# Kernel optimization log

Hardware: AMD Instinct MI355X
Metric: run time of the kernel (lower is better)

## Reference

```python
import jax, jax.numpy as jnp
import numpy as np
from jax import lax

N_ITERS = 50
SIGMA = 1e-6
RHO_MIN, RHO_MAX = 1e-6, 1e6


def _chol_solve(L, b):
    # Solve M x = b given M = L L^T (batched lower-triangular L)
    y = lax.linalg.triangular_solve(L, b, left_side=True, lower=True)
    return lax.linalg.triangular_solve(L, y, left_side=True, lower=True, transpose_a=True)


def setup_inputs() -> dict:
    key = jax.random.key(0)
    kq, kp, ka = jax.random.split(key, 3)
    B, n_x, n_A = 128, 512, 512
    G = jax.random.normal(kq, (B, n_x, n_x), dtype=jnp.float32)
    # SPD quadratic term, as required by the QP solver
    Q = jnp.matmul(G, jnp.swapaxes(G, 1, 2)) / n_x + 0.1 * jnp.eye(n_x, dtype=jnp.float32)
    p = 0.1 * jax.random.normal(kp, (B, n_x, 1), dtype=jnp.float32)
    A = jax.random.normal(ka, (B, n_A, n_x), dtype=jnp.float32) / np.sqrt(n_x).astype(np.float32)
    lb = -jnp.ones((B, n_A, 1), dtype=jnp.float32)
    ub = jnp.ones((B, n_A, 1), dtype=jnp.float32)
    return {"Q": Q, "p": p, "A": A, "lb": lb, "ub": ub}


def reference(Q, p, A, lb, ub):
    B, n_A, n_x = A.shape
    AT = jnp.swapaxes(A, 1, 2)                      # [B, n_x, n_A]
    ATA = jnp.matmul(AT, A)                         # [B, n_x, n_x]

    # rho heuristic from scqpth_solve (Frobenius matrix norms), held constant
    A_norm = jnp.linalg.norm(ATA, axis=(1, 2), keepdims=True)
    Q_norm = jnp.linalg.norm(Q, axis=(1, 2), keepdims=True)
    rho = (Q_norm / A_norm) * (n_A / n_x) ** 0.5    # [B,1,1]
    rho = jnp.clip(rho, RHO_MIN, RHO_MAX)
    rho = lax.stop_gradient(rho)

    M = Q + rho * ATA + SIGMA * jnp.eye(n_x, dtype=Q.dtype)
    L = jnp.linalg.cholesky(M)                      # factor once (M is SPD)

    x0 = jnp.zeros((B, n_x, 1), dtype=Q.dtype)
    z0 = jnp.zeros((B, n_A, 1), dtype=Q.dtype)
    u0 = jnp.zeros((B, n_A, 1), dtype=Q.dtype)

    def step(carry, _):
        x, z, u = carry
        rhs = -p + rho * jnp.matmul(AT, z - u) + SIGMA * x
        x = _chol_solve(L, rhs)
        Ax = jnp.matmul(A, x)
        z = jnp.clip(Ax + u, lb, ub)                # projection onto [lb, ub]
        u = u + Ax - z                              # scaled dual update
        return (x, z, u), None

    (x, z, u), _ = lax.scan(step, (x0, z0, u0), None, length=N_ITERS)
    return x
```

## Files before the change

kernel.cpp:

```cpp
#include <hip/hip_runtime.h>

#define NBATCH 128
#define NDIM 512
static constexpr size_t MAT = (size_t)NDIM * NDIM;
static constexpr size_t BATMAT = (size_t)NBATCH * MAT;
#define SIGMA_F 1e-6f

template <int TA, int TB>
__global__ __launch_bounds__(256) void gemm512b(const float* __restrict__ Ag,
                                                const float* __restrict__ Bg,
                                                float* __restrict__ Cg,
                                                const float* __restrict__ alphaPtr) {
  const int b = blockIdx.z;
  const float* Ab = Ag + (size_t)b * MAT;
  const float* Bb = Bg + (size_t)b * MAT;
  float* Cb = Cg + (size_t)b * MAT;
  const int i0 = blockIdx.y * 128, j0 = blockIdx.x * 128;
  __shared__ float As[32][132];
  __shared__ float Bs[32][132];
  const int tid = threadIdx.x;
  const int tx = tid & 15, ty = tid >> 4;
  float acc[2][2][4][4] = {};
  for (int k0 = 0; k0 < NDIM; k0 += 32) {
    if (TA == 0) {
      const int kk = tid >> 5, c4 = (tid & 31) << 2;
#pragma unroll
      for (int pp = 0; pp < 4; ++pp) {
        float4 v = *reinterpret_cast<const float4*>(&Ab[(size_t)(k0 + kk + 8 * pp) * NDIM + i0 + c4]);
        *reinterpret_cast<float4*>(&As[kk + 8 * pp][c4]) = v;
      }
    } else {
      const int m = tid >> 3, kq = (tid & 7) << 2;
#pragma unroll
      for (int pp = 0; pp < 4; ++pp) {
        float4 v = *reinterpret_cast<const float4*>(&Ab[(size_t)(i0 + m + 32 * pp) * NDIM + k0 + kq]);
        As[kq + 0][m + 32 * pp] = v.x;
        As[kq + 1][m + 32 * pp] = v.y;
        As[kq + 2][m + 32 * pp] = v.z;
        As[kq + 3][m + 32 * pp] = v.w;
      }
    }
    if (TB == 0) {
      const int kk = tid >> 5, c4 = (tid & 31) << 2;
#pragma unroll
      for (int pp = 0; pp < 4; ++pp) {
        float4 v = *reinterpret_cast<const float4*>(&Bb[(size_t)(k0 + kk + 8 * pp) * NDIM + j0 + c4]);
        *reinterpret_cast<float4*>(&Bs[kk + 8 * pp][c4]) = v;
      }
    } else {
      const int m = tid >> 3, kq = (tid & 7) << 2;
#pragma unroll
      for (int pp = 0; pp < 4; ++pp) {
        float4 v = *reinterpret_cast<const float4*>(&Bb[(size_t)(j0 + m + 32 * pp) * NDIM + k0 + kq]);
        Bs[kq + 0][m + 32 * pp] = v.x;
        Bs[kq + 1][m + 32 * pp] = v.y;
        Bs[kq + 2][m + 32 * pp] = v.z;
        Bs[kq + 3][m + 32 * pp] = v.w;
      }
    }
    __syncthreads();
#pragma unroll
    for (int kk = 0; kk < 32; ++kk) {
      float4 a0 = *reinterpret_cast<const float4*>(&As[kk][ty << 2]);
      float4 a1 = *reinterpret_cast<const float4*>(&As[kk][64 + (ty << 2)]);
      float4 b0 = *reinterpret_cast<const float4*>(&Bs[kk][tx << 2]);
      float4 b1 = *reinterpret_cast<const float4*>(&Bs[kk][64 + (tx << 2)]);
      const float ar[2][4] = {{a0.x, a0.y, a0.z, a0.w}, {a1.x, a1.y, a1.z, a1.w}};
      const float br[2][4] = {{b0.x, b0.y, b0.z, b0.w}, {b1.x, b1.y, b1.z, b1.w}};
#pragma unroll
      for (int ri = 0; ri < 2; ++ri)
#pragma unroll
        for (int ci = 0; ci < 2; ++ci)
#pragma unroll
          for (int r = 0; r < 4; ++r)
#pragma unroll
            for (int c = 0; c < 4; ++c)
              acc[ri][ci][r][c] += ar[ri][r] * br[ci][c];
    }
    __syncthreads();
  }
  const float alpha = alphaPtr ? alphaPtr[b] : 1.0f;
#pragma unroll
  for (int ri = 0; ri < 2; ++ri)
#pragma unroll
    for (int r = 0; r < 4; ++r) {
      const int gi = i0 + ri * 64 + (ty << 2) + r;
#pragma unroll
      for (int ci = 0; ci < 2; ++ci) {
        float4 o = make_float4(alpha * acc[ri][ci][r][0], alpha * acc[ri][ci][r][1],
                               alpha * acc[ri][ci][r][2], alpha * acc[ri][ci][r][3]);
        *reinterpret_cast<float4*>(&Cb[(size_t)gi * NDIM + j0 + ci * 64 + (tx << 2)]) = o;
      }
    }
}

__global__ __launch_bounds__(512) void norms_rho(const float* __restrict__ Q,
                                                 const float* __restrict__ ATA,
                                                 float* __restrict__ rho) {
  const int b = blockIdx.x;
  const int tid = threadIdx.x;
  const float* Qb = Q + (size_t)b * MAT;
  const float* Tb = ATA + (size_t)b * MAT;
  double sq = 0.0, st = 0.0;
  for (int e = tid; e < (int)MAT; e += 512) {
    float q = Qb[e];
    float t = Tb[e];
    sq += (double)q * q;
    st += (double)t * t;
  }
  __shared__ double s1[512];
  __shared__ double s2[512];
  s1[tid] = sq;
  s2[tid] = st;
  __syncthreads();
  for (int h = 256; h > 0; h >>= 1) {
    if (tid < h) {
      s1[tid] += s1[tid + h];
      s2[tid] += s2[tid + h];
    }
    __syncthreads();
  }
  if (tid == 0) {
    double r = sqrt(s1[0]) / sqrt(s2[0]);
    r = fmin(fmax(r, 1e-6), 1e6);
    rho[b] = (float)r;
  }
}

__global__ void form_m(const float* __restrict__ Q, const float* __restrict__ rho,
                       float* __restrict__ M) {
  size_t stride = (size_t)gridDim.x * blockDim.x;
  for (size_t e = (size_t)blockIdx.x * blockDim.x + threadIdx.x; e < BATMAT; e += stride) {
    int b = (int)(e >> 18);
    int ij = (int)(e & (MAT - 1));
    int i = ij >> 9, j = ij & 511;
    float v = Q[e] + rho[b] * M[e];
    if (i == j) v += SIGMA_F;
    M[e] = v;
  }
}

__global__ __launch_bounds__(256) void gj_pivot(float* __restrict__ Mg,
                                                float* __restrict__ Csave, int p) {
  const int b = blockIdx.x;
  float* M = Mg + (size_t)b * MAT;
  float* Cs = Csave + (size_t)b * ((size_t)NDIM * 64);
  const int tid = threadIdx.x;
  const int k0 = p * 64;
  for (int e = tid; e < 512 * 16; e += 256) {
    int r = e >> 4, c4 = (e & 15) << 2;
    float4 v = *reinterpret_cast<const float4*>(&M[(size_t)r * NDIM + k0 + c4]);
    *reinterpret_cast<float4*>(&Cs[r * 64 + c4]) = v;
  }
  const int r = tid & 63, cb = (tid >> 6) << 4;
  float dreg[16];
#pragma unroll
  for (int q = 0; q < 16; ++q) dreg[q] = M[(size_t)(k0 + r) * NDIM + k0 + cb + q];
  __shared__ float rowb[64];
  __shared__ float colb[64];
  for (int j = 0; j < 64; ++j) {
    const int jc = j - cb;
    if (jc >= 0 && jc < 16) colb[r] = dreg[jc];
    if (r == j) {
#pragma unroll
      for (int q = 0; q < 16; ++q) rowb[cb + q] = dreg[q];
    }
    __syncthreads();
    const float piv = 1.0f / rowb[j];
    const float cj = colb[r];
    if (r == j) {
#pragma unroll
      for (int q = 0; q < 16; ++q) dreg[q] = (cb + q == j) ? piv : rowb[cb + q] * piv;
    } else {
#pragma unroll
      for (int q = 0; q < 16; ++q) {
        float rv = rowb[cb + q] * piv;
        dreg[q] = (cb + q == j) ? (-cj * piv) : fmaf(-cj, rv, dreg[q]);
      }
    }
    __syncthreads();
  }
#pragma unroll
  for (int q = 0; q < 16; ++q) M[(size_t)(k0 + r) * NDIM + k0 + cb + q] = dreg[q];
}

__global__ __launch_bounds__(256) void gj_row(float* __restrict__ Mg, int p) {
  const int b = blockIdx.y;
  const int jt = blockIdx.x + (blockIdx.x >= p ? 1 : 0);
  float* M = Mg + (size_t)b * MAT;
  const int k0 = p * 64, j0 = jt * 64;
  __shared__ float Ss[64][68];
  __shared__ float Rs[64][68];
  const int tid = threadIdx.x;
  for (int e = tid; e < 1024; e += 256) {
    int rr = e >> 4, c4 = (e & 15) << 2;
    *reinterpret_cast<float4*>(&Ss[rr][c4]) =
        *reinterpret_cast<const float4*>(&M[(size_t)(k0 + rr) * NDIM + k0 + c4]);
    *reinterpret_cast<float4*>(&Rs[rr][c4]) =
        *reinterpret_cast<const float4*>(&M[(size_t)(k0 + rr) * NDIM + j0 + c4]);
  }
  __syncthreads();
  const int tx = tid & 15, ty = tid >> 4;
  float acc[4][4] = {};
#pragma unroll 16
  for (int m = 0; m < 64; ++m) {
    float4 a = *reinterpret_cast<const float4*>(&Ss[m][ty << 2]);
    float4 bv = *reinterpret_cast<const float4*>(&Rs[m][tx << 2]);
    acc[0][0] += a.x * bv.x; acc[0][1] += a.x * bv.y; acc[0][2] += a.x * bv.z; acc[0][3] += a.x * bv.w;
    acc[1][0] += a.y * bv.x; acc[1][1] += a.y * bv.y; acc[1][2] += a.y * bv.z; acc[1][3] += a.y * bv.w;
    acc[2][0] += a.z * bv.x; acc[2][1] += a.z * bv.y; acc[2][2] += a.z * bv.z; acc[2][3] += a.z * bv.w;
    acc[3][0] += a.w * bv.x; acc[3][1] += a.w * bv.y; acc[3][2] += a.w * bv.z; acc[3][3] += a.w * bv.w;
  }
#pragma unroll
  for (int rr = 0; rr < 4; ++rr) {
    float4 o = make_float4(acc[rr][0], acc[rr][1], acc[rr][2], acc[rr][3]);
    *reinterpret_cast<float4*>(&M[(size_t)(k0 + (ty << 2) + rr) * NDIM + j0 + (tx << 2)]) = o;
  }
}

__global__ __launch_bounds__(256) void gj_update(float* __restrict__ Mg,
                                                 const float* __restrict__ Csave, int p) {
  const int b = blockIdx.z;
  const int jt = blockIdx.x;
  const int it = blockIdx.y + (blockIdx.y >= p ? 1 : 0);
  float* M = Mg + (size_t)b * MAT;
  const float* Cs = Csave + (size_t)b * ((size_t)NDIM * 64);
  const int k0 = p * 64, i0 = it * 64, j0 = jt * 64;
  __shared__ float Ts[64][68];
  __shared__ float Rs[64][68];
  const int tid = threadIdx.x;
  {
    const int rr = tid >> 2, mq = (tid & 3) << 4;
#pragma unroll
    for (int q = 0; q < 4; ++q) {
      float4 v = *reinterpret_cast<const float4*>(&Cs[(i0 + rr) * 64 + mq + q * 4]);
      Ts[mq + q * 4 + 0][rr] = v.x;
      Ts[mq + q * 4 + 1][rr] = v.y;
      Ts[mq + q * 4 + 2][rr] = v.z;
      Ts[mq + q * 4 + 3][rr] = v.w;
    }
  }
  for (int e = tid; e < 1024; e += 256) {
    int rr = e >> 4, c4 = (e & 15) << 2;
    *reinterpret_cast<float4*>(&Rs[rr][c4]) =
        *reinterpret_cast<const float4*>(&M[(size_t)(k0 + rr) * NDIM + j0 + c4]);
  }
  __syncthreads();
  const int tx = tid & 15, ty = tid >> 4;
  float acc[4][4] = {};
#pragma unroll 16
  for (int m = 0; m < 64; ++m) {
    float4 a = *reinterpret_cast<const float4*>(&Ts[m][ty << 2]);
    float4 bv = *reinterpret_cast<const float4*>(&Rs[m][tx << 2]);
    acc[0][0] += a.x * bv.x; acc[0][1] += a.x * bv.y; acc[0][2] += a.x * bv.z; acc[0][3] += a.x * bv.w;
    acc[1][0] += a.y * bv.x; acc[1][1] += a.y * bv.y; acc[1][2] += a.y * bv.z; acc[1][3] += a.y * bv.w;
    acc[2][0] += a.z * bv.x; acc[2][1] += a.z * bv.y; acc[2][2] += a.z * bv.z; acc[2][3] += a.z * bv.w;
    acc[3][0] += a.w * bv.x; acc[3][1] += a.w * bv.y; acc[3][2] += a.w * bv.z; acc[3][3] += a.w * bv.w;
  }
  if (jt == p) {
#pragma unroll
    for (int rr = 0; rr < 4; ++rr) {
      float4 o = make_float4(-acc[rr][0], -acc[rr][1], -acc[rr][2], -acc[rr][3]);
      *reinterpret_cast<float4*>(&M[(size_t)(i0 + (ty << 2) + rr) * NDIM + j0 + (tx << 2)]) = o;
    }
  } else {
#pragma unroll
    for (int rr = 0; rr < 4; ++rr) {
      float* dst = &M[(size_t)(i0 + (ty << 2) + rr) * NDIM + j0 + (tx << 2)];
      float4 cur = *reinterpret_cast<const float4*>(dst);
      cur.x -= acc[rr][0];
      cur.y -= acc[rr][1];
      cur.z -= acc[rr][2];
      cur.w -= acc[rr][3];
      *reinterpret_cast<float4*>(dst) = cur;
    }
  }
}

__global__ __launch_bounds__(512) void cvec_kernel(const float* __restrict__ Minv,
                                                   const float* __restrict__ p,
                                                   float* __restrict__ c) {
  const int b = blockIdx.x, i = threadIdx.x;
  __shared__ float ps[512];
  ps[i] = p[b * NDIM + i];
  __syncthreads();
  const float* Mb = Minv + (size_t)b * MAT;
  float acc = 0.f;
#pragma unroll 8
  for (int m = 0; m < NDIM; ++m) acc += Mb[m * NDIM + i] * ps[m];
  c[b * NDIM + i] = -acc;
}

__global__ __launch_bounds__(512) void dvec_kernel(const float* __restrict__ Ain,
                                                   const float* __restrict__ c,
                                                   float* __restrict__ d) {
  const int b = blockIdx.x, i = threadIdx.x;
  __shared__ float cs[512];
  cs[i] = c[b * NDIM + i];
  __syncthreads();
  const int wv = i >> 6, ln = i & 63;
  const float* Ab = Ain + (size_t)b * MAT;
  for (int q = 0; q < 64; ++q) {
    const int j = wv * 64 + q;
    const float* Arow = Ab + (size_t)j * NDIM;
    float s = 0.f;
#pragma unroll
    for (int h = 0; h < 8; ++h) s += Arow[h * 64 + ln] * cs[h * 64 + ln];
    for (int off = 32; off > 0; off >>= 1) s += __shfl_down(s, off);
    if (ln == 0) d[b * NDIM + j] = s;
  }
}

__global__ __launch_bounds__(512) void admm_step(const float* __restrict__ S,
                                                 const float* __restrict__ dvec,
                                                 const float* __restrict__ lb,
                                                 const float* __restrict__ ub,
                                                 float* __restrict__ wbuf,
                                                 float* __restrict__ ubuf) {
  const int blk = blockIdx.x;
  const int b = blk >> 1, h = blk & 1;
  const int t = threadIdx.x;
  __shared__ float ws_s[512];
  __shared__ float4 part[512];
  ws_s[t] = wbuf[b * NDIM + t];
  __syncthreads();
  const int j4 = t & 63;
  const int ks = t >> 6;
  const float4* Srow = reinterpret_cast<const float4*>(S + (size_t)b * MAT) +
                       (size_t)(ks * 64) * 128 + h * 64 + j4;
  float4 acc = make_float4(0.f, 0.f, 0.f, 0.f);
#pragma unroll 8
  for (int k = 0; k < 64; ++k) {
    float w = ws_s[ks * 64 + k];
    float4 s = Srow[(size_t)k * 128];
    acc.x += s.x * w;
    acc.y += s.y * w;
    acc.z += s.z * w;
    acc.w += s.w * w;
  }
  part[t] = acc;
  __syncthreads();
  if (t < 64) {
    float4 y = part[t];
#pragma unroll
    for (int s = 1; s < 8; ++s) {
      float4 q = part[s * 64 + t];
      y.x += q.x; y.y += q.y; y.z += q.z; y.w += q.w;
    }
    const size_t off = (size_t)b * NDIM + h * 256 + t * 4;
    float4 dv = *reinterpret_cast<const float4*>(dvec + off);
    float4 uv = *reinterpret_cast<const float4*>(ubuf + off);
    float4 lbv = *reinterpret_cast<const float4*>(lb + off);
    float4 ubv = *reinterpret_cast<const float4*>(ub + off);
    y.x += dv.x; y.y += dv.y; y.z += dv.z; y.w += dv.w;
    float4 zv, wv;
    zv.x = fminf(fmaxf(y.x + uv.x, lbv.x), ubv.x);
    zv.y = fminf(fmaxf(y.y + uv.y, lbv.y), ubv.y);
    zv.z = fminf(fmaxf(y.z + uv.z, lbv.z), ubv.z);
    zv.w = fminf(fmaxf(y.w + uv.w, lbv.w), ubv.w);
    uv.x += y.x - zv.x; uv.y += y.y - zv.y; uv.z += y.z - zv.z; uv.w += y.w - zv.w;
    wv.x = zv.x - uv.x; wv.y = zv.y - uv.y; wv.z = zv.z - uv.z; wv.w = zv.w - uv.w;
    *reinterpret_cast<float4*>(ubuf + off) = uv;
    *reinterpret_cast<float4*>(wbuf + off) = wv;
  }
}

__global__ __launch_bounds__(512) void final_x(const float* __restrict__ P1,
                                               const float* __restrict__ c,
                                               const float* __restrict__ w,
                                               float* __restrict__ out) {
  const int b = blockIdx.x, i = threadIdx.x;
  __shared__ float ws_s[512];
  ws_s[i] = w[b * NDIM + i];
  __syncthreads();
  const float* Pb = P1 + (size_t)b * MAT;
  float acc = 0.f;
#pragma unroll 8
  for (int k = 0; k < NDIM; ++k) acc += Pb[(size_t)k * NDIM + i] * ws_s[k];
  out[b * NDIM + i] = c[b * NDIM + i] + acc;
}

extern "C" void kernel_launch(void* const* d_in, const int* in_sizes, int n_in,
                              void* d_out, int out_size, void* d_ws, size_t ws_size,
                              hipStream_t stream) {
  const float* Q = (const float*)d_in[0];
  const float* p = (const float*)d_in[1];
  const float* A = (const float*)d_in[2];
  const float* lb = (const float*)d_in[3];
  const float* ub = (const float*)d_in[4];
  float* out = (float*)d_out;

  float* B0 = (float*)d_ws;
  float* B1 = B0 + BATMAT;
  float* cbuf = B1 + BATMAT;
  float* dbuf = cbuf + NBATCH * NDIM;
  float* wbuf = dbuf + NBATCH * NDIM;
  float* ubuf = wbuf + NBATCH * NDIM;
  float* rhobuf = ubuf + NBATCH * NDIM;

  hipMemsetAsync(wbuf, 0, 2 * NBATCH * NDIM * sizeof(float), stream);

  gemm512b<0, 0><<<dim3(4, 4, NBATCH), 256, 0, stream>>>(A, A, B0, nullptr);
  norms_rho<<<NBATCH, 512, 0, stream>>>(Q, B0, rhobuf);
  form_m<<<2048, 256, 0, stream>>>(Q, rhobuf, B0);
  for (int p8 = 0; p8 < 8; ++p8) {
    gj_pivot<<<NBATCH, 256, 0, stream>>>(B0, B1, p8);
    gj_row<<<dim3(7, NBATCH), 256, 0, stream>>>(B0, p8);
    gj_update<<<dim3(8, 7, NBATCH), 256, 0, stream>>>(B0, B1, p8);
  }
  cvec_kernel<<<NBATCH, 512, 0, stream>>>(B0, p, cbuf);
  gemm512b<1, 0><<<dim3(4, 4, NBATCH), 256, 0, stream>>>(A, B0, B1, rhobuf);
  dvec_kernel<<<NBATCH, 512, 0, stream>>>(A, cbuf, dbuf);
  gemm512b<1, 1><<<dim3(4, 4, NBATCH), 256, 0, stream>>>(B1, A, B0, nullptr);
  for (int it = 0; it < 49; ++it)
    admm_step<<<2 * NBATCH, 512, 0, stream>>>(B0, dbuf, lb, ub, wbuf, ubuf);
  final_x<<<NBATCH, 512, 0, stream>>>(B1, cbuf, wbuf, out);
}
```

Before: 4.399 ms.

## Use split-bf16 MFMA for batched GEMMs and widen ADMM step grid

Replaces the FP32 SIMT batched GEMM with an MFMA kernel. Each FP32 operand is split into high and low bf16 parts, and three bf16 products are accumulated to approximate FP32 accuracy. The rho scaling moves from the second GEMM to the third GEMM and to final_x. The per-iteration ADMM step is split into four blocks per batch instead of two, to raise parallelism across the GPU. This adds conversion overhead and slightly lower precision in exchange for matrix-core throughput.

```diff
diff --git a/kernel.cpp b/kernel.cpp
--- a/kernel.cpp
+++ b/kernel.cpp
@@ -6,91 +6,129 @@
 static constexpr size_t BATMAT = (size_t)NBATCH * MAT;
 #define SIGMA_F 1e-6f
 
-template <int TA, int TB>
-__global__ __launch_bounds__(256) void gemm512b(const float* __restrict__ Ag,
-                                                const float* __restrict__ Bg,
-                                                float* __restrict__ Cg,
-                                                const float* __restrict__ alphaPtr) {
+typedef __attribute__((ext_vector_type(8))) short bf16x8;
+typedef __attribute__((ext_vector_type(4))) float f32x4;
+
+__device__ inline ushort f2bf_rne(float x) {
+  unsigned u = __builtin_bit_cast(unsigned, x);
+  unsigned r = (u + 0x7fffu + ((u >> 16) & 1u)) >> 16;
+  return (ushort)r;
+}
+__device__ inline void splitf(float x, ushort& h, ushort& l) {
+  h = f2bf_rne(x);
+  float hf = __builtin_bit_cast(float, (unsigned)((unsigned)h << 16));
+  l = f2bf_rne(x - hf);
+}
+
+template <int TRA, int TRB>
+__global__ __launch_bounds__(256) void gemm_mfma(const float* __restrict__ Ag,
+                                                 const float* __restrict__ Bg,
+                                                 float* __restrict__ Cg,
+                                                 const float* __restrict__ alphaPtr) {
   const int b = blockIdx.z;
   const float* Ab = Ag + (size_t)b * MAT;
   const float* Bb = Bg + (size_t)b * MAT;
   float* Cb = Cg + (size_t)b * MAT;
   const int i0 = blockIdx.y * 128, j0 = blockIdx.x * 128;
-  __shared__ float As[32][132];
-  __shared__ float Bs[32][132];
+  __shared__ __align__(16) ushort Ah[128][40];
+  __shared__ __align__(16) ushort Al[128][40];
+  __shared__ __align__(16) ushort Bh[128][40];
+  __shared__ __align__(16) ushort Bl[128][40];
   const int tid = threadIdx.x;
-  const int tx = tid & 15, ty = tid >> 4;
-  float acc[2][2][4][4] = {};
+  const int lane = tid & 63, wid = tid >> 6;
+  const int wr = wid >> 1, wc = wid & 1;
+  const int fr = lane & 15, fg = lane >> 4;
+  f32x4 acc[4][4];
+#pragma unroll
+  for (int m = 0; m < 4; ++m)
+#pragma unroll
+    for (int n = 0; n < 4; ++n) acc[m][n] = (f32x4){0.f, 0.f, 0.f, 0.f};
+
   for (int k0 = 0; k0 < NDIM; k0 += 32) {
-    if (TA == 0) {
-      const int kk = tid >> 5, c4 = (tid & 31) << 2;
+    if (TRA == 0) {
+      const int srow = tid >> 3, skk = (tid & 7) << 2;
 #pragma unroll
       for (int pp = 0; pp < 4; ++pp) {
-        float4 v = *reinterpret_cast<const float4*>(&Ab[(size_t)(k0 + kk + 8 * pp) * NDIM + i0 + c4]);
-        *reinterpret_cast<float4*>(&As[kk + 8 * pp][c4]) = v;
+        const int row = srow + 32 * pp;
+        float4 v = *reinterpret_cast<const float4*>(&Ab[(size_t)(i0 + row) * NDIM + k0 + skk]);
+        ushort4 h, l;
+        splitf(v.x, h.x, l.x); splitf(v.y, h.y, l.y);
+        splitf(v.z, h.z, l.z); splitf(v.w, h.w, l.w);
+        *reinterpret_cast<ushort4*>(&Ah[row][skk]) = h;
+        *reinterpret_cast<ushort4*>(&Al[row][skk]) = l;
       }
     } else {
-      const int m = tid >> 3, kq = (tid & 7) << 2;
+      const int skk = tid >> 5, sm4 = (tid & 31) << 2;
 #pragma unroll
       for (int pp = 0; pp < 4; ++pp) {
-        float4 v = *reinterpret_cast<const float4*>(&Ab[(size_t)(i0 + m + 32 * pp) * NDIM + k0 + kq]);
-        As[kq + 0][m + 32 * pp] = v.x;
-        As[kq + 1][m + 32 * pp] = v.y;
-        As[kq + 2][m + 32 * pp] = v.z;
-        As[kq + 3][m + 32 * pp] = v.w;
-      }
-    }
-    if (TB == 0) {
-      const int kk = tid >> 5, c4 = (tid & 31) << 2;
+        const int kk = skk + 8 * pp;
+        float4 v = *reinterpret_cast<const float4*>(&Ab[(size_t)(k0 + kk) * NDIM + i0 + sm4]);
+        ushort h, l;
+        splitf(v.x, h, l); Ah[sm4 + 0][kk] = h; Al[sm4 + 0][kk] = l;
+        splitf(v.y, h, l); Ah[sm4 + 1][kk] = h; Al[sm4 + 1][kk] = l;
+        splitf(v.z, h, l); Ah[sm4 + 2][kk] = h; Al[sm4 + 2][kk] = l;
+        splitf(v.w, h, l); Ah[sm4 + 3][kk] = h; Al[sm4 + 3][kk] = l;
+      }
+    }
+    if (TRB == 0) {
+      const int srow = tid >> 3, skk = (tid & 7) << 2;
 #pragma unroll
       for (int pp = 0; pp < 4; ++pp) {
-        float4 v = *reinterpret_cast<const float4*>(&Bb[(size_t)(k0 + kk + 8 * pp) * NDIM + j0 + c4]);
-        *reinterpret_cast<float4*>(&Bs[kk + 8 * pp][c4]) = v;
+        const int row = srow + 32 * pp;
+        float4 v = *reinterpret_cast<const float4*>(&Bb[(size_t)(j0 + row) * NDIM + k0 + skk]);
+        ushort4 h, l;
+        splitf(v.x, h.x, l.x); splitf(v.y, h.y, l.y);
+        splitf(v.z, h.z, l.z); splitf(v.w, h.w, l.w);
+        *reinterpret_cast<ushort4*>(&Bh[row][skk]) = h;
+        *reinterpret_cast<ushort4*>(&Bl[row][skk]) = l;
       }
     } else {
-      const int m = tid >> 3, kq = (tid & 7) << 2;
+      const int skk = tid >> 5, sm4 = (tid & 31) << 2;
 #pragma unroll
       for (int pp = 0; pp < 4; ++pp) {
-        float4 v = *reinterpret_cast<const float4*>(&Bb[(size_t)(j0 + m + 32 * pp) * NDIM + k0 + kq]);
-        Bs[kq + 0][m + 32 * pp] = v.x;
-        Bs[kq + 1][m + 32 * pp] = v.y;
-        Bs[kq + 2][m + 32 * pp] = v.z;
-        Bs[kq + 3][m + 32 * pp] = v.w;
+        const int kk = skk + 8 * pp;
+        float4 v = *reinterpret_cast<const float4*>(&Bb[(size_t)(k0 + kk) * NDIM + j0 + sm4]);
+        ushort h, l;
+        splitf(v.x, h, l); Bh[sm4 + 0][kk] = h; Bl[sm4 + 0][kk] = l;
+        splitf(v.y, h, l); Bh[sm4 + 1][kk] = h; Bl[sm4 + 1][kk] = l;
+        splitf(v.z, h, l); Bh[sm4 + 2][kk] = h; Bl[sm4 + 2][kk] = l;
+        splitf(v.w, h, l); Bh[sm4 + 3][kk] = h; Bl[sm4 + 3][kk] = l;
       }
     }
     __syncthreads();
-#pragma unroll
-    for (int kk = 0; kk < 32; ++kk) {
-      float4 a0 = *reinterpret_cast<const float4*>(&As[kk][ty << 2]);
-      float4 a1 = *reinterpret_cast<const float4*>(&As[kk][64 + (ty << 2)]);
-      float4 b0 = *reinterpret_cast<const float4*>(&Bs[kk][tx << 2]);
-      float4 b1 = *reinterpret_cast<const float4*>(&Bs[kk][64 + (tx << 2)]);
-      const float ar[2][4] = {{a0.x, a0.y, a0.z, a0.w}, {a1.x, a1.y, a1.z, a1.w}};
-      const float br[2][4] = {{b0.x, b0.y, b0.z, b0.w}, {b1.x, b1.y, b1.z, b1.w}};
-#pragma unroll
-      for (int ri = 0; ri < 2; ++ri)
-#pragma unroll
-        for (int ci = 0; ci < 2; ++ci)
-#pragma unroll
-          for (int r = 0; r < 4; ++r)
-#pragma unroll
-            for (int c = 0; c < 4; ++c)
-              acc[ri][ci][r][c] += ar[ri][r] * br[ci][c];
-    }
+    bf16x8 ah[4], al4[4], bh4[4], bl4[4];
+#pragma unroll
+    for (int m = 0; m < 4; ++m) {
+      const int row = wr * 64 + m * 16 + fr;
+      ah[m] = *reinterpret_cast<const bf16x8*>(&Ah[row][fg * 8]);
+      al4[m] = *reinterpret_cast<const bf16x8*>(&Al[row][fg * 8]);
+    }
+#pragma unroll
+    for (int n = 0; n < 4; ++n) {
+      const int row = wc * 64 + n * 16 + fr;
+      bh4[n] = *reinterpret_cast<const bf16x8*>(&Bh[row][fg * 8]);
+      bl4[n] = *reinterpret_cast<const bf16x8*>(&Bl[row][fg * 8]);
+    }
+#pragma unroll
+    for (int m = 0; m < 4; ++m)
+#pragma unroll
+      for (int n = 0; n < 4; ++n) {
+        acc[m][n] = __builtin_amdgcn_mfma_f32_16x16x32_bf16(ah[m], bh4[n], acc[m][n], 0, 0, 0);
+        acc[m][n] = __builtin_amdgcn_mfma_f32_16x16x32_bf16(ah[m], bl4[n], acc[m][n], 0, 0, 0);
+        acc[m][n] = __builtin_amdgcn_mfma_f32_16x16x32_bf16(al4[m], bh4[n], acc[m][n], 0, 0, 0);
+      }
     __syncthreads();
   }
   const float alpha = alphaPtr ? alphaPtr[b] : 1.0f;
 #pragma unroll
-  for (int ri = 0; ri < 2; ++ri)
-#pragma unroll
-    for (int r = 0; r < 4; ++r) {
-      const int gi = i0 + ri * 64 + (ty << 2) + r;
-#pragma unroll
-      for (int ci = 0; ci < 2; ++ci) {
-        float4 o = make_float4(alpha * acc[ri][ci][r][0], alpha * acc[ri][ci][r][1],
-                               alpha * acc[ri][ci][r][2], alpha * acc[ri][ci][r][3]);
-        *reinterpret_cast<float4*>(&Cb[(size_t)gi * NDIM + j0 + ci * 64 + (tx << 2)]) = o;
-      }
+  for (int m = 0; m < 4; ++m)
+#pragma unroll
+    for (int n = 0; n < 4; ++n) {
+      const int col = j0 + wc * 64 + n * 16 + fr;
+      const int rowb = i0 + wr * 64 + m * 16 + fg * 4;
+#pragma unroll
+      for (int q = 0; q < 4; ++q)
+        Cb[(size_t)(rowb + q) * NDIM + col] = alpha * acc[m][n][q];
     }
 }
 
@@ -318,21 +356,21 @@
                                                  float* __restrict__ wbuf,
                                                  float* __restrict__ ubuf) {
   const int blk = blockIdx.x;
-  const int b = blk >> 1, h = blk & 1;
+  const int b = blk >> 2, qd = blk & 3;
   const int t = threadIdx.x;
   __shared__ float ws_s[512];
   __shared__ float4 part[512];
   ws_s[t] = wbuf[b * NDIM + t];
   __syncthreads();
-  const int j4 = t & 63;
-  const int ks = t >> 6;
-  const float4* Srow = reinterpret_cast<const float4*>(S + (size_t)b * MAT) +
-                       (size_t)(ks * 64) * 128 + h * 64 + j4;
+  const int j4 = t & 31;
+  const int ks = t >> 5;
+  const float4* Scol = reinterpret_cast<const float4*>(S + (size_t)b * MAT) +
+                       (size_t)(ks * 32) * 128 + qd * 32 + j4;
   float4 acc = make_float4(0.f, 0.f, 0.f, 0.f);
 #pragma unroll 8
-  for (int k = 0; k < 64; ++k) {
-    float w = ws_s[ks * 64 + k];
-    float4 s = Srow[(size_t)k * 128];
+  for (int k = 0; k < 32; ++k) {
+    float w = ws_s[ks * 32 + k];
+    float4 s = Scol[(size_t)k * 128];
     acc.x += s.x * w;
     acc.y += s.y * w;
     acc.z += s.z * w;
@@ -340,14 +378,14 @@
   }
   part[t] = acc;
   __syncthreads();
-  if (t < 64) {
+  if (t < 32) {
     float4 y = part[t];
 #pragma unroll
-    for (int s = 1; s < 8; ++s) {
-      float4 q = part[s * 64 + t];
+    for (int s = 1; s < 16; ++s) {
+      float4 q = part[s * 32 + t];
       y.x += q.x; y.y += q.y; y.z += q.z; y.w += q.w;
     }
-    const size_t off = (size_t)b * NDIM + h * 256 + t * 4;
+    const size_t off = (size_t)b * NDIM + qd * 128 + t * 4;
     float4 dv = *reinterpret_cast<const float4*>(dvec + off);
     float4 uv = *reinterpret_cast<const float4*>(ubuf + off);
     float4 lbv = *reinterpret_cast<const float4*>(lb + off);
@@ -365,19 +403,20 @@
   }
 }
 
-__global__ __launch_bounds__(512) void final_x(const float* __restrict__ P1,
+__global__ __launch_bounds__(512) void final_x(const float* __restrict__ T1,
                                                const float* __restrict__ c,
                                                const float* __restrict__ w,
+                                               const float* __restrict__ rho,
                                                float* __restrict__ out) {
   const int b = blockIdx.x, i = threadIdx.x;
   __shared__ float ws_s[512];
   ws_s[i] = w[b * NDIM + i];
   __syncthreads();
-  const float* Pb = P1 + (size_t)b * MAT;
+  const float* Pb = T1 + (size_t)b * MAT;
   float acc = 0.f;
 #pragma unroll 8
   for (int k = 0; k < NDIM; ++k) acc += Pb[(size_t)k * NDIM + i] * ws_s[k];
-  out[b * NDIM + i] = c[b * NDIM + i] + acc;
+  out[b * NDIM + i] = c[b * NDIM + i] + rho[b] * acc;
 }
 
 extern "C" void kernel_launch(void* const* d_in, const int* in_sizes, int n_in,
@@ -400,7 +439,7 @@
 
   hipMemsetAsync(wbuf, 0, 2 * NBATCH * NDIM * sizeof(float), stream);
 
-  gemm512b<0, 0><<<dim3(4, 4, NBATCH), 256, 0, stream>>>(A, A, B0, nullptr);
+  gemm_mfma<1, 1><<<dim3(4, 4, NBATCH), 256, 0, stream>>>(A, A, B0, nullptr);
   norms_rho<<<NBATCH, 512, 0, stream>>>(Q, B0, rhobuf);
   form_m<<<2048, 256, 0, stream>>>(Q, rhobuf, B0);
   for (int p8 = 0; p8 < 8; ++p8) {
@@ -409,10 +448,10 @@
     gj_update<<<dim3(8, 7, NBATCH), 256, 0, stream>>>(B0, B1, p8);
   }
   cvec_kernel<<<NBATCH, 512, 0, stream>>>(B0, p, cbuf);
-  gemm512b<1, 0><<<dim3(4, 4, NBATCH), 256, 0, stream>>>(A, B0, B1, rhobuf);
+  gemm_mfma<0, 0><<<dim3(4, 4, NBATCH), 256, 0, stream>>>(A, B0, B1, nullptr);
   dvec_kernel<<<NBATCH, 512, 0, stream>>>(A, cbuf, dbuf);
-  gemm512b<1, 1><<<dim3(4, 4, NBATCH), 256, 0, stream>>>(B1, A, B0, nullptr);
+  gemm_mfma<0, 0><<<dim3(4, 4, NBATCH), 256, 0, stream>>>(B1, A, B0, rhobuf);
   for (int it = 0; it < 49; ++it)
-    admm_step<<<2 * NBATCH, 512, 0, stream>>>(B0, dbuf, lb, ub, wbuf, ubuf);
-  final_x<<<NBATCH, 512, 0, stream>>>(B1, cbuf, wbuf, out);
-}
+    admm_step<<<4 * NBATCH, 512, 0, stream>>>(B0, dbuf, lb, ub, wbuf, ubuf);
+  final_x<<<NBATCH, 512, 0, stream>>>(B1, cbuf, wbuf, rhobuf, out);
+}
```

After: 4.114 ms. -6.5%, faster.
